# Kernel tuning notes

Measured on AMD Instinct MI355X. Metric: run time of the kernel, lower is better.

Reference implementation:

```python
import jax, jax.numpy as jnp
import numpy as np

B, IN, COND, H, LAT, E, GH = 8192, 256, 1024, 1024, 128, 6, 64
INP = LAT + COND      # decoder layer0 input size = 1152
INTER = LAT + H       # decoder layer1/2 input size = 1152


def setup_inputs() -> dict:
    key = jax.random.key(0)
    ks = jax.random.split(key, 30)
    n = lambda k, shape, s=0.02: jax.random.normal(k, shape, dtype=jnp.float32) * s
    return {
        'x': jax.random.normal(ks[0], (B, IN), dtype=jnp.float32),
        'y': jax.random.normal(ks[1], (B, COND), dtype=jnp.float32),
        'eps': jax.random.normal(ks[2], (B, LAT), dtype=jnp.float32),
        # encoder: layer k input = prev_dim + IN (x is re-concatenated each layer)
        'enc_w0': n(ks[3], (IN + COND + IN, H)), 'enc_b0': jnp.zeros((H,), jnp.float32),
        'enc_w1': n(ks[4], (H + IN, H)),         'enc_b1': jnp.zeros((H,), jnp.float32),
        'mu_w': n(ks[5], (H, LAT)),  'mu_b': jnp.zeros((LAT,), jnp.float32),
        'lv_w': n(ks[6], (H, LAT)),  'lv_b': jnp.zeros((LAT,), jnp.float32),
        # gating network (input = latent + cond)
        'g_w0': n(ks[7], (INP, GH)), 'g_b0': jnp.zeros((GH,), jnp.float32),
        'g_w1': n(ks[8], (GH, GH)),  'g_b1': jnp.zeros((GH,), jnp.float32),
        'g_w2': n(ks[9], (GH, E)),   'g_b2': jnp.zeros((E,), jnp.float32),
        # expert weights [E, in, out] and biases [E, out] (bias init 0.01 as in source)
        'exp_w0': n(ks[10], (E, INP, H)),   'exp_b0': jnp.full((E, H), 0.01, jnp.float32),
        'exp_w1': n(ks[11], (E, INTER, H)), 'exp_b1': jnp.full((E, H), 0.01, jnp.float32),
        'exp_w2': n(ks[12], (E, INTER, IN)), 'exp_b2': jnp.full((E, IN), 0.01, jnp.float32),
    }


def _forward(x, y, eps, enc_w0, enc_b0, enc_w1, enc_b1, mu_w, mu_b, lv_w, lv_b,
             g_w0, g_b0, g_w1, g_b1, g_w2, g_b2,
             exp_w0, exp_b0, exp_w1, exp_b1, exp_w2, exp_b2):
    elu = jax.nn.elu
    # --- Encoder ---
    h = jnp.concatenate([x, y], axis=1)
    h = elu(jnp.concatenate([h, x], axis=1) @ enc_w0 + enc_b0)
    h = elu(jnp.concatenate([h, x], axis=1) @ enc_w1 + enc_b1)
    mu = h @ mu_w + mu_b
    logvar = h @ lv_w + lv_b
    # --- Reparameterize (eps passed explicitly for determinism) ---
    z = mu + eps * jnp.exp(0.5 * logvar)
    # --- MixedDecoder ---
    g = jnp.concatenate([z, y], axis=1)
    g = elu(g @ g_w0 + g_b0)
    g = elu(g @ g_w1 + g_b1)
    coeff = jax.nn.softmax(g @ g_w2 + g_b2, axis=1)  # [B, E]
    layer_out = y
    for W, bb, act in ((exp_w0, exp_b0, True), (exp_w1, exp_b1, True), (exp_w2, exp_b2, False)):
        inp = jnp.concatenate([z, layer_out], axis=1)  # [B, I]
        # fused mixture-of-experts projection: avoids materializing per-sample [B,I,O] weight
        out = coeff @ bb + jnp.einsum('be,bi,eio->bo', coeff, inp, W)
        layer_out = elu(out) if act else out
    return layer_out, mu, logvar


def reference(x, y, eps, enc_w0, enc_b0, enc_w1, enc_b1, mu_w, mu_b, lv_w, lv_b,
              g_w0, g_b0, g_w1, g_b1, g_w2, g_b2,
              exp_w0, exp_b0, exp_w1, exp_b1, exp_w2, exp_b2):
    return _forward(x, y, eps, enc_w0, enc_b0, enc_w1, enc_b1, mu_w, mu_b, lv_w, lv_b,
                    g_w0, g_b0, g_w1, g_b1, g_w2, g_b2,
                    exp_w0, exp_b0, exp_w1, exp_b1, exp_w2, exp_b2)
```

## Files before the change

### kernel.cpp

```cpp
#include <hip/hip_runtime.h>
#include <hip/hip_bf16.h>
#include <cstddef>

using u16 = unsigned short;
using short8 = __attribute__((ext_vector_type(8))) short;
using f32x4 = __attribute__((ext_vector_type(4))) float;

constexpr int B_   = 8192;
constexpr int IN_  = 256;
constexpr int COND_= 1024;
constexpr int H_   = 1024;
constexpr int LAT_ = 128;
constexpr int NE_  = 6;
constexpr int GH_  = 64;
constexpr int INP_ = 1152;
constexpr int K0_  = 1536;
constexpr int K1_  = 1280;

constexpr int BK = 64;

typedef const __attribute__((address_space(1))) void gv_t;
typedef __attribute__((address_space(3))) void lv_t;
#define GLDS(g, l) __builtin_amdgcn_global_load_lds((gv_t*)(g), (lv_t*)(l), 16, 0, 0)

__device__ __forceinline__ u16 f2b(float f) {
  __hip_bfloat16 h = __float2bfloat16(f);
  return *reinterpret_cast<u16*>(&h);
}
__device__ __forceinline__ ushort4 f2b4(float4 v) {
  ushort4 o;
  o.x = f2b(v.x); o.y = f2b(v.y); o.z = f2b(v.z); o.w = f2b(v.w);
  return o;
}
__device__ __forceinline__ float elu1(float x) { return x > 0.f ? x : (__expf(x) - 1.f); }

__global__ void k_transpose(const float* __restrict__ in, u16* __restrict__ out,
                            int R, int C, long inStride, long outStride) {
  __shared__ float t[32][33];
  const float* ip = in + (long)blockIdx.z * inStride;
  u16* op = out + (long)blockIdx.z * outStride;
  int c0 = blockIdx.x * 32, r0 = blockIdx.y * 32;
  int tx = threadIdx.x, ty = threadIdx.y;
#pragma unroll
  for (int i = 0; i < 4; i++) {
    int r = r0 + ty + i * 8, c = c0 + tx;
    if (r < R && c < C) t[ty + i * 8][tx] = ip[(long)r * C + c];
  }
  __syncthreads();
#pragma unroll
  for (int i = 0; i < 4; i++) {
    int c = c0 + ty + i * 8, r = r0 + tx;
    if (r < R && c < C) op[(long)c * R + r] = f2b(t[tx][ty + i * 8]);
  }
}

__global__ __launch_bounds__(256) void k_pre(
    const float* __restrict__ enc_w0, const float* __restrict__ enc_w1,
    const float* __restrict__ mu_w, const float* __restrict__ lv_w,
    const float* __restrict__ g_w0, const float* __restrict__ exp_w0,
    const float* __restrict__ exp_w1,
    const float* __restrict__ x, const float* __restrict__ y,
    u16* __restrict__ encw0T, u16* __restrict__ encw1T, u16* __restrict__ mulvT,
    u16* __restrict__ gw0T, u16* __restrict__ ew0T, u16* __restrict__ ew1T,
    u16* __restrict__ A0, u16* __restrict__ A1, int pbase)
{
  __shared__ float t[32][33];
  const int b = blockIdx.x;
  const int tid = threadIdx.x;
  const int tx = tid & 31, ty = tid >> 5;

  auto tr = [&](const float* in, u16* out, int R, int C, int bx, int by) {
    int c0 = bx * 32, r0 = by * 32;
#pragma unroll
    for (int i = 0; i < 4; i++) {
      int r = r0 + ty + i * 8, c = c0 + tx;
      if (r < R && c < C) t[ty + i * 8][tx] = in[(long)r * C + c];
    }
    __syncthreads();
#pragma unroll
    for (int i = 0; i < 4; i++) {
      int c = c0 + ty + i * 8, r = r0 + tx;
      if (r < R && c < C) out[(long)c * R + r] = f2b(t[tx][ty + i * 8]);
    }
  };

  if (b < 1536)       { tr(enc_w0, encw0T, K0_, H_, b & 31, b >> 5); }
  else if (b < 2816)  { int l = b - 1536; tr(enc_w1, encw1T, K1_, H_, l & 31, l >> 5); }
  else if (b < 2944)  { int l = b - 2816; tr(mu_w, mulvT, H_, LAT_, l & 3, l >> 2); }
  else if (b < 3072)  { int l = b - 2944; tr(lv_w, mulvT + (size_t)LAT_ * H_, H_, LAT_, l & 3, l >> 2); }
  else if (b < 3144)  { int l = b - 3072; tr(g_w0, gw0T, INP_, GH_, l & 1, l >> 1); }
  else if (b < 10056) {
    int l = b - 3144, e = l / 1152, r2 = l % 1152;
    tr(exp_w0 + (long)e * INP_ * H_, ew0T + (long)e * INP_ * H_, INP_, H_, r2 & 31, r2 >> 5);
  } else if (b < pbase) {
    int l = b - 10056, e = l / 1152, r2 = l % 1152;
    tr(exp_w1 + (long)e * INP_ * H_, ew1T + (long)e * INP_ * H_, INP_, H_, r2 & 31, r2 >> 5);
  } else {
    long idx = (long)(b - pbase) * 256 + tid;
    long n0v = (long)B_ * K0_ / 4;
    if (idx < n0v) {
      long base = idx * 4;
      int bb = (int)(base / K0_), c = (int)(base % K0_);
      float4 v;
      if (c < IN_)              v = *(const float4*)&x[(long)bb * IN_ + c];
      else if (c < IN_ + COND_) v = *(const float4*)&y[(long)bb * COND_ + (c - IN_)];
      else                      v = *(const float4*)&x[(long)bb * IN_ + (c - IN_ - COND_)];
      *(ushort4*)&A0[base] = f2b4(v);
    } else {
      long j = idx - n0v;
      if (j < (long)B_ * IN_ / 4) {
        long base = j * 4;
        int bb = (int)(base / IN_), c = (int)(base % IN_);
        float4 v = *(const float4*)&x[(long)bb * IN_ + c];
        *(ushort4*)&A1[(long)bb * K1_ + H_ + c] = f2b4(v);
      }
    }
  }
}

__global__ __launch_bounds__(256) void k_mid(
    const float* __restrict__ exp_w2, u16* __restrict__ ew2T,
    const float* __restrict__ mu, const float* __restrict__ lv,
    const float* __restrict__ eps, const float* __restrict__ y,
    u16* __restrict__ ZY, u16* __restrict__ D1, u16* __restrict__ D2)
{
  __shared__ float t[32][33];
  const int b = blockIdx.x;
  const int tid = threadIdx.x;
  if (b < 1728) {
    const int tx = tid & 31, ty = tid >> 5;
    int e = b / 288, r2 = b % 288;
    const float* in = exp_w2 + (long)e * INP_ * IN_;
    u16* out = ew2T + (long)e * INP_ * IN_;
    int c0 = (r2 & 7) * 32, r0 = (r2 >> 3) * 32;
#pragma unroll
    for (int i = 0; i < 4; i++) {
      int r = r0 + ty + i * 8, c = c0 + tx;
      if (r < INP_ && c < IN_) t[ty + i * 8][tx] = in[(long)r * IN_ + c];
    }
    __syncthreads();
#pragma unroll
    for (int i = 0; i < 4; i++) {
      int c = c0 + ty + i * 8, r = r0 + tx;
      if (r < INP_ && c < IN_) out[(long)c * INP_ + r] = f2b(t[tx][ty + i * 8]);
    }
  } else {
    long idx = (long)(b - 1728) * 256 + tid;
    if (idx >= (long)B_ * INP_ / 4) return;
    long base = idx * 4;
    int bb = (int)(base / INP_), c = (int)(base % INP_);
    if (c < LAT_) {
      long o = (long)bb * LAT_ + c;
      float4 m = *(const float4*)&mu[o];
      float4 l = *(const float4*)&lv[o];
      float4 e4 = *(const float4*)&eps[o];
      float4 z;
      z.x = m.x + e4.x * __expf(0.5f * l.x);
      z.y = m.y + e4.y * __expf(0.5f * l.y);
      z.z = m.z + e4.z * __expf(0.5f * l.z);
      z.w = m.w + e4.w * __expf(0.5f * l.w);
      ushort4 zb = f2b4(z);
      *(ushort4*)&ZY[base] = zb;
      *(ushort4*)&D1[base] = zb;
      *(ushort4*)&D2[base] = zb;
    } else {
      float4 v = *(const float4*)&y[(long)bb * COND_ + (c - LAT_)];
      *(ushort4*)&ZY[base] = f2b4(v);
    }
  }
}

__global__ __launch_bounds__(256) void k_gate(const float* __restrict__ G1,
    const float* __restrict__ w1, const float* __restrict__ b1,
    const float* __restrict__ w2, const float* __restrict__ b2,
    float* __restrict__ coeff) {
  __shared__ float W1[64][65];
  __shared__ float W2[64][8];
  __shared__ float B1[64], B2[8];
  int tid = threadIdx.x;
  for (int i = tid; i < 64 * 64; i += 256) W1[i >> 6][i & 63] = w1[i];
  for (int i = tid; i < 64 * 6; i += 256) W2[i / 6][i % 6] = w2[i];
  if (tid < 64) B1[tid] = b1[tid];
  if (tid < 8)  B2[tid] = (tid < 6) ? b2[tid] : 0.f;
  __syncthreads();
  int row = blockIdx.x * 256 + tid;
  const float* gr = G1 + (long)row * GH_;
  float g[64];
#pragma unroll
  for (int i = 0; i < 16; i++) {
    float4 v = *(const float4*)(gr + i * 4);
    g[i*4] = v.x; g[i*4+1] = v.y; g[i*4+2] = v.z; g[i*4+3] = v.w;
  }
  float lg[6];
#pragma unroll
  for (int e = 0; e < 6; e++) lg[e] = B2[e];
  for (int n = 0; n < 64; n++) {
    float s = B1[n];
#pragma unroll
    for (int k = 0; k < 64; k++) s += g[k] * W1[k][n];
    s = elu1(s);
#pragma unroll
    for (int e = 0; e < 6; e++) lg[e] += s * W2[n][e];
  }
  float m = lg[0];
#pragma unroll
  for (int e = 1; e < 6; e++) m = fmaxf(m, lg[e]);
  float p[6], sum = 0.f;
#pragma unroll
  for (int e = 0; e < 6; e++) { p[e] = __expf(lg[e] - m); sum += p[e]; }
  float inv = 1.f / sum;
#pragma unroll
  for (int e = 0; e < 6; e++) coeff[(long)row * 6 + e] = p[e] * inv;
}

template<int KSTEPS, int E, bool MOE>
__global__ __launch_bounds__(512, 2) void k_gemm8(
    const u16* __restrict__ A,
    const u16* __restrict__ WT,
    const float* __restrict__ bias,
    const float* __restrict__ coeff,
    int N,
    u16* __restrict__ outH, int ldo)
{
  constexpr int KK = KSTEPS * BK;
  constexpr int T = E * KSTEPS;
  __shared__ __align__(16) u16 As[3][256][BK];
  __shared__ __align__(16) u16 Bs[3][128][BK];
  __shared__ float Cf[MOE ? 256 : 1][8];

  const int tid = threadIdx.x;
  const int lane = tid & 63, w = tid >> 6;
  const int wr = w >> 1, wc = w & 1;
  const int lin = blockIdx.x + blockIdx.y * gridDim.x;
  const int rb  = (lin & 7) * 4 + ((lin >> 3) & 3);
  const int cp  = lin >> 5;
  const int brow = rb * 256, bcol = cp * 128;
  const int lr = lane & 15, hi = lane >> 4;
  const int lk = hi * 8;
  const int xsw = (lr & 7) << 3;

  if (MOE) {
    if (tid < 256) {
#pragma unroll
      for (int e2 = 0; e2 < 8; e2++)
        Cf[tid][e2] = (e2 < 6) ? coeff[(long)(brow + tid) * 6 + e2] : 0.f;
    }
    __syncthreads();
  }

  f32x4 acc[4][4];
#pragma unroll
  for (int m = 0; m < 4; m++)
#pragma unroll
    for (int n = 0; n < 4; n++)
#pragma unroll
      for (int r = 0; r < 4; r++) acc[m][n][r] = 0.f;
  f32x4 pacc[MOE ? 4 : 1][MOE ? 4 : 1];
  if constexpr (MOE) {
#pragma unroll
    for (int m = 0; m < 4; m++)
#pragma unroll
      for (int n = 0; n < 4; n++)
#pragma unroll
        for (int r = 0; r < 4; r++) pacc[m][n][r] = 0.f;
  }

  const int srow = w * 8 + (lane >> 3);
  const int sdst = (lane & 7) * 8;
  const int ssrc = ((lane & 7) ^ ((lane >> 3) & 7)) * 8;
  const u16* Asrc = A + (long)(brow + srow) * KK + ssrc;
  const u16* Bsrc = WT + (long)(bcol + srow) * KK + ssrc;

  auto STAGE_H = [&](int t2, int buf, int h) {
    const int e2 = (E == 1) ? 0 : (t2 / KSTEPS);
    int k2 = (E == 1) ? t2 : (t2 % KSTEPS);
    if (E > 1 && (e2 & 1)) k2 = KSTEPS - 1 - k2;
    const u16* ap = Asrc + (long)k2 * BK;
    const u16* bp = Bsrc + (long)e2 * ((long)N * KK) + (long)k2 * BK;
    GLDS(ap + (long)((h * 2 + 0) * 64) * KK, &As[buf][(h * 2 + 0) * 64 + srow][sdst]);
    GLDS(ap + (long)((h * 2 + 1) * 64) * KK, &As[buf][(h * 2 + 1) * 64 + srow][sdst]);
    GLDS(bp + (long)(h * 64) * KK,           &Bs[buf][h * 64 + srow][sdst]);
  };

  STAGE_H(0, 0, 0); STAGE_H(0, 0, 1);
  STAGE_H(1, 1, 0); STAGE_H(1, 1, 1);
  asm volatile("s_waitcnt vmcnt(6)" ::: "memory");
  asm volatile("s_barrier" ::: "memory");

  for (int t = 0; t < T; ++t) {
    const int cur = t % 3;
    const int nbuf = (t + 2) % 3;
    const bool do_stage = (t + 2 < T);

    {
      short8 af[4], bfr[4];
      const int cc = lk ^ xsw;
#pragma unroll
      for (int m = 0; m < 4; m++)
        af[m] = *(const short8*)&As[cur][wr * 64 + m * 16 + lr][cc];
#pragma unroll
      for (int n = 0; n < 4; n++)
        bfr[n] = *(const short8*)&Bs[cur][wc * 64 + n * 16 + lr][cc];
      if (do_stage) STAGE_H(t + 2, nbuf, 0);
      asm volatile("s_barrier" ::: "memory");
      __builtin_amdgcn_s_setprio(1);
#pragma unroll
      for (int m = 0; m < 4; m++)
#pragma unroll
        for (int n = 0; n < 4; n++) {
          if constexpr (MOE)
            pacc[m][n] = __builtin_amdgcn_mfma_f32_16x16x32_bf16(af[m], bfr[n], pacc[m][n], 0, 0, 0);
          else
            acc[m][n] = __builtin_amdgcn_mfma_f32_16x16x32_bf16(af[m], bfr[n], acc[m][n], 0, 0, 0);
        }
      __builtin_amdgcn_s_setprio(0);
      asm volatile("s_barrier" ::: "memory");
    }

    {
      short8 af[4], bfr[4];
      const int cc = (32 + lk) ^ xsw;
#pragma unroll
      for (int m = 0; m < 4; m++)
        af[m] = *(const short8*)&As[cur][wr * 64 + m * 16 + lr][cc];
#pragma unroll
      for (int n = 0; n < 4; n++)
        bfr[n] = *(const short8*)&Bs[cur][wc * 64 + n * 16 + lr][cc];
      if (do_stage) STAGE_H(t + 2, nbuf, 1);
      asm volatile("s_barrier" ::: "memory");
      __builtin_amdgcn_s_setprio(1);
#pragma unroll
      for (int m = 0; m < 4; m++)
#pragma unroll
        for (int n = 0; n < 4; n++) {
          if constexpr (MOE)
            pacc[m][n] = __builtin_amdgcn_mfma_f32_16x16x32_bf16(af[m], bfr[n], pacc[m][n], 0, 0, 0);
          else
            acc[m][n] = __builtin_amdgcn_mfma_f32_16x16x32_bf16(af[m], bfr[n], acc[m][n], 0, 0, 0);
        }
      __builtin_amdgcn_s_setprio(0);
      if (t + 1 < T) {
        if (do_stage) asm volatile("s_waitcnt vmcnt(6)" ::: "memory");
        else          asm volatile("s_waitcnt vmcnt(0)" ::: "memory");
      }
      asm volatile("s_barrier" ::: "memory");
    }

    if constexpr (MOE) {
      if ((t + 1) % KSTEPS == 0) {
        const int e = t / KSTEPS;
#pragma unroll
        for (int m = 0; m < 4; m++)
#pragma unroll
          for (int r = 0; r < 4; r++) {
            float c = Cf[wr * 64 + m * 16 + hi * 4 + r][e];
#pragma unroll
            for (int n = 0; n < 4; n++) acc[m][n][r] += c * pacc[m][n][r];
          }
        if (t + 1 < T) {
#pragma unroll
          for (int m = 0; m < 4; m++)
#pragma unroll
            for (int n = 0; n < 4; n++)
#pragma unroll
              for (int r = 0; r < 4; r++) pacc[m][n][r] = 0.f;
        }
      }
    }
  }

#pragma unroll
  for (int m = 0; m < 4; m++)
#pragma unroll
    for (int n = 0; n < 4; n++) {
      const int col = bcol + wc * 64 + n * 16 + lr;
#pragma unroll
      for (int r = 0; r < 4; r++) {
        const int rowl = wr * 64 + m * 16 + hi * 4 + r;
        const long row = brow + rowl;
        float v = acc[m][n][r];
        if constexpr (MOE) {
          float bv = 0.f;
#pragma unroll
          for (int e = 0; e < 6; e++) bv += Cf[rowl][e] * bias[(long)e * N + col];
          v += bv;
        } else {
          v += bias[col];
        }
        v = elu1(v);
        outH[row * (long)ldo + col] = f2b(v);
      }
    }
}

template<int KSTEPS, int E, bool MOE>
__global__ __launch_bounds__(256, 2) void k_m2(
    const u16* __restrict__ A,
    const u16* __restrict__ WT,
    const float* __restrict__ bias, const float* __restrict__ bias2,
    const float* __restrict__ coeff,
    int N,
    u16* __restrict__ outH, float* __restrict__ outF, float* __restrict__ outF2,
    int ldo, int splitcol, int act)
{
  constexpr int KK = KSTEPS * BK;
  constexpr int T = E * KSTEPS;
  __shared__ __align__(16) u16 As[3][64][BK];
  __shared__ __align__(16) u16 Bs[3][128][BK];
  __shared__ float Cf[MOE ? 64 : 1][8];

  const int tid = threadIdx.x;
  const int lane = tid & 63, w = tid >> 6;
  const int wr = w >> 1, wc = w & 1;
  const int brow = blockIdx.x * 64, bcol = blockIdx.y * 128;
  const int lr = lane & 15, hi = lane >> 4;
  const int lk = hi * 8;
  const int xsw = (lr & 7) << 3;

  if (MOE) {
    if (tid < 64) {
#pragma unroll
      for (int e2 = 0; e2 < 8; e2++)
        Cf[tid][e2] = (e2 < 6) ? coeff[(long)(brow + tid) * 6 + e2] : 0.f;
    }
    __syncthreads();
  }

  f32x4 acc[2][4];
#pragma unroll
  for (int m = 0; m < 2; m++)
#pragma unroll
    for (int n = 0; n < 4; n++)
#pragma unroll
      for (int r = 0; r < 4; r++) acc[m][n][r] = 0.f;
  f32x4 pacc[MOE ? 2 : 1][MOE ? 4 : 1];
  if constexpr (MOE) {
#pragma unroll
    for (int m = 0; m < 2; m++)
#pragma unroll
      for (int n = 0; n < 4; n++)
#pragma unroll
        for (int r = 0; r < 4; r++) pacc[m][n][r] = 0.f;
  }

  const int srow = w * 8 + (lane >> 3);
  const int sdst = (lane & 7) * 8;
  const int ssrc = ((lane & 7) ^ ((lane >> 3) & 7)) * 8;
  const u16* Asrc = A + (long)(brow + srow) * KK + ssrc;
  const u16* Bsrc = WT + (long)(bcol + srow) * KK + ssrc;

  auto STAGE_H = [&](int t2, int buf, int h) {
    const int e2 = (E == 1) ? 0 : (t2 / KSTEPS);
    int k2 = (E == 1) ? t2 : (t2 % KSTEPS);
    if (E > 1 && (e2 & 1)) k2 = KSTEPS - 1 - k2;
    const u16* ap = Asrc + (long)k2 * BK;
    const u16* bp = Bsrc + (long)e2 * ((long)N * KK) + (long)k2 * BK;
    GLDS(ap + (long)(h * 32) * KK,            &As[buf][h * 32 + srow][sdst]);
    GLDS(bp + (long)(h * 64) * KK,            &Bs[buf][h * 64 + srow][sdst]);
    GLDS(bp + (long)(h * 64 + 32) * KK,       &Bs[buf][h * 64 + 32 + srow][sdst]);
  };

  STAGE_H(0, 0, 0); STAGE_H(0, 0, 1);
  STAGE_H(1, 1, 0); STAGE_H(1, 1, 1);
  asm volatile("s_waitcnt vmcnt(6)" ::: "memory");
  asm volatile("s_barrier" ::: "memory");

  for (int t = 0; t < T; ++t) {
    const int cur = t % 3;
    const int nbuf = (t + 2) % 3;
    const bool do_stage = (t + 2 < T);

    {
      short8 af[2], bfr[4];
      const int cc = lk ^ xsw;
#pragma unroll
      for (int m = 0; m < 2; m++)
        af[m] = *(const short8*)&As[cur][wr * 32 + m * 16 + lr][cc];
#pragma unroll
      for (int n = 0; n < 4; n++)
        bfr[n] = *(const short8*)&Bs[cur][wc * 64 + n * 16 + lr][cc];
      if (do_stage) STAGE_H(t + 2, nbuf, 0);
      asm volatile("s_barrier" ::: "memory");
      __builtin_amdgcn_s_setprio(1);
#pragma unroll
      for (int m = 0; m < 2; m++)
#pragma unroll
        for (int n = 0; n < 4; n++) {
          if constexpr (MOE)
            pacc[m][n] = __builtin_amdgcn_mfma_f32_16x16x32_bf16(af[m], bfr[n], pacc[m][n], 0, 0, 0);
          else
            acc[m][n] = __builtin_amdgcn_mfma_f32_16x16x32_bf16(af[m], bfr[n], acc[m][n], 0, 0, 0);
        }
      __builtin_amdgcn_s_setprio(0);
      asm volatile("s_barrier" ::: "memory");
    }
    {
      short8 af[2], bfr[4];
      const int cc = (32 + lk) ^ xsw;
#pragma unroll
      for (int m = 0; m < 2; m++)
        af[m] = *(const short8*)&As[cur][wr * 32 + m * 16 + lr][cc];
#pragma unroll
      for (int n = 0; n < 4; n++)
        bfr[n] = *(const short8*)&Bs[cur][wc * 64 + n * 16 + lr][cc];
      if (do_stage) STAGE_H(t + 2, nbuf, 1);
      asm volatile("s_barrier" ::: "memory");
      __builtin_amdgcn_s_setprio(1);
#pragma unroll
      for (int m = 0; m < 2; m++)
#pragma unroll
        for (int n = 0; n < 4; n++) {
          if constexpr (MOE)
            pacc[m][n] = __builtin_amdgcn_mfma_f32_16x16x32_bf16(af[m], bfr[n], pacc[m][n], 0, 0, 0);
          else
            acc[m][n] = __builtin_amdgcn_mfma_f32_16x16x32_bf16(af[m], bfr[n], acc[m][n], 0, 0, 0);
        }
      __builtin_amdgcn_s_setprio(0);
      if (t + 1 < T) {
        if (do_stage) asm volatile("s_waitcnt vmcnt(6)" ::: "memory");
        else          asm volatile("s_waitcnt vmcnt(0)" ::: "memory");
      }
      asm volatile("s_barrier" ::: "memory");
    }

    if constexpr (MOE) {
      if ((t + 1) % KSTEPS == 0) {
        const int e = t / KSTEPS;
#pragma unroll
        for (int m = 0; m < 2; m++)
#pragma unroll
          for (int r = 0; r < 4; r++) {
            float c = Cf[wr * 32 + m * 16 + hi * 4 + r][e];
#pragma unroll
            for (int n = 0; n < 4; n++) acc[m][n][r] += c * pacc[m][n][r];
          }
        if (t + 1 < T) {
#pragma unroll
          for (int m = 0; m < 2; m++)
#pragma unroll
            for (int n = 0; n < 4; n++)
#pragma unroll
              for (int r = 0; r < 4; r++) pacc[m][n][r] = 0.f;
        }
      }
    }
  }

#pragma unroll
  for (int m = 0; m < 2; m++)
#pragma unroll
    for (int n = 0; n < 4; n++) {
      const int col = bcol + wc * 64 + n * 16 + lr;
      if (col >= N) continue;
#pragma unroll
      for (int r = 0; r < 4; r++) {
        const int rowl = wr * 32 + m * 16 + hi * 4 + r;
        const long row = brow + rowl;
        float v = acc[m][n][r];
        if constexpr (MOE) {
          float bv = 0.f;
#pragma unroll
          for (int e = 0; e < 6; e++) bv += Cf[rowl][e] * bias[(long)e * N + col];
          v += bv;
        } else {
          v += (col < splitcol) ? bias[col] : bias2[col - splitcol];
        }
        if (act) v = elu1(v);
        if (outH) outH[row * (long)ldo + col] = f2b(v);
        else if (col < splitcol) outF[row * (long)ldo + col] = v;
        else outF2[row * (long)ldo + (col - splitcol)] = v;
      }
    }
}

extern "C" void kernel_launch(void* const* d_in, const int* in_sizes, int n_in,
                              void* d_out, int out_size, void* d_ws, size_t ws_size,
                              hipStream_t stream) {
  (void)in_sizes; (void)out_size;
  if (n_in < 23) return;
  const float* x      = (const float*)d_in[0];
  const float* y      = (const float*)d_in[1];
  const float* eps    = (const float*)d_in[2];
  const float* enc_w0 = (const float*)d_in[3];
  const float* enc_b0 = (const float*)d_in[4];
  const float* enc_w1 = (const float*)d_in[5];
  const float* enc_b1 = (const float*)d_in[6];
  const float* mu_w   = (const float*)d_in[7];
  const float* mu_b   = (const float*)d_in[8];
  const float* lv_w   = (const float*)d_in[9];
  const float* lv_b   = (const float*)d_in[10];
  const float* g_w0   = (const float*)d_in[11];
  const float* g_b0   = (const float*)d_in[12];
  const float* g_w1   = (const float*)d_in[13];
  const float* g_b1   = (const float*)d_in[14];
  const float* g_w2   = (const float*)d_in[15];
  const float* g_b2   = (const float*)d_in[16];
  const float* exp_w0 = (const float*)d_in[17];
  const float* exp_b0 = (const float*)d_in[18];
  const float* exp_w1 = (const float*)d_in[19];
  const float* exp_b1 = (const float*)d_in[20];
  const float* exp_w2 = (const float*)d_in[21];
  const float* exp_b2 = (const float*)d_in[22];

  char* ws = (char*)d_ws;
  size_t off = 0;
  auto alloc = [&](size_t bytes) -> void* {
    void* p = ws + off; off += (bytes + 255) & ~(size_t)255; return p;
  };
  u16* A0     = (u16*)alloc((size_t)B_ * K0_ * 2);
  u16* A1     = (u16*)alloc((size_t)B_ * K1_ * 2);
  u16* H2     = (u16*)alloc((size_t)B_ * H_ * 2);
  u16* ZY     = (u16*)alloc((size_t)B_ * INP_ * 2);
  u16* encw0T = (u16*)alloc((size_t)K0_ * H_ * 2);
  u16* encw1T = (u16*)alloc((size_t)K1_ * H_ * 2);
  u16* mulvT  = (u16*)alloc((size_t)256 * H_ * 2);
  u16* gw0T   = (u16*)alloc((size_t)GH_ * INP_ * 2);
  u16* ew0T   = (u16*)alloc((size_t)NE_ * H_ * INP_ * 2);
  if (ws_size < off) return;

  size_t ew1_bytes = (size_t)NE_ * H_ * INP_ * 2;
  u16* ew1T_sep = nullptr;
  if (off + ew1_bytes <= ws_size) ew1T_sep = (u16*)alloc(ew1_bytes);

  u16* D1 = A0;
  u16* D2 = A1;
  float* G1    = (float*)H2;
  float* COEFF = (float*)((char*)H2 + (size_t)B_ * GH_ * 4);
  u16* ew2T = (u16*)((char*)H2 + (size_t)4 * 1024 * 1024);
  u16* ew1T = ew1T_sep ? ew1T_sep : ZY;

  float* outO = (float*)d_out;
  float* muO  = outO + (size_t)B_ * IN_;
  float* lvO  = muO + (size_t)B_ * LAT_;

  const int hoist = ew1T_sep ? 1 : 0;
  const int pbase = hoist ? 16968 : 10056;
  const int pre_grid = pbase + 14336;

  k_pre<<<pre_grid, 256, 0, stream>>>(enc_w0, enc_w1, mu_w, lv_w, g_w0, exp_w0,
      exp_w1, x, y, encw0T, encw1T, mulvT, gw0T, ew0T, ew1T, A0, A1, pbase);

  k_gemm8<K0_ / BK, 1, false><<<dim3(32, 8), 512, 0, stream>>>(A0, encw0T, enc_b0,
      nullptr, H_, A1, K1_);
  k_gemm8<K1_ / BK, 1, false><<<dim3(32, 8), 512, 0, stream>>>(A1, encw1T, enc_b1,
      nullptr, H_, H2, H_);

  k_m2<H_ / BK, 1, false><<<dim3(B_ / 64, 2), 256, 0, stream>>>(H2, mulvT,
      mu_b, lv_b, nullptr, 256, nullptr, muO, lvO, LAT_, LAT_, 0);

  k_mid<<<10944, 256, 0, stream>>>(exp_w2, ew2T, muO, lvO, eps, y, ZY, D1, D2);

  k_m2<INP_ / BK, 1, false><<<dim3(B_ / 64, 1), 256, 0, stream>>>(ZY, gw0T,
      g_b0, g_b0, nullptr, GH_, nullptr, G1, nullptr, GH_, GH_, 1);
  k_gate<<<B_ / 256, 256, 0, stream>>>(G1, g_w1, g_b1, g_w2, g_b2, COEFF);

  k_gemm8<INP_ / BK, NE_, true><<<dim3(32, 8), 512, 0, stream>>>(ZY, ew0T, exp_b0,
      COEFF, H_, D1 + LAT_, INP_);
  if (!hoist) {
    k_transpose<<<dim3(32, 36, NE_), dim3(32, 8), 0, stream>>>(exp_w1, ew1T, INP_, H_,
                                                      (long)INP_ * H_, (long)INP_ * H_);
  }
  k_gemm8<INP_ / BK, NE_, true><<<dim3(32, 8), 512, 0, stream>>>(D1, ew1T, exp_b1,
      COEFF, H_, D2 + LAT_, INP_);
  k_m2<INP_ / BK, NE_, true><<<dim3(B_ / 64, 2), 256, 0, stream>>>(D2, ew2T,
      exp_b2, nullptr, COEFF, IN_, nullptr, outO, nullptr, IN_, IN_, 0);
}
```

Measured before the change: 521.6 us.

## Add dedicated MoE GEMM kernel with k-outer expert-inner loop and A-tile reuse

Introduces k_moe4, a 256-thread kernel with 128x128 tiles for the two large mixture-of-experts layers. The loop runs over K outermost and all six experts inside, so one A tile is loaded into shared memory once and reused across experts. Each expert's partial product is scaled by its gate coefficient and added to the accumulator at every K step. This removes the repeated A reloads per expert in the old expert-outer order, at the cost of more per-step coefficient FMAs, smaller tiles and more blocks. The encoder GEMM is simplified to a non-MoE-only template.

```diff
diff --git a/kernel.cpp b/kernel.cpp
--- a/kernel.cpp
+++ b/kernel.cpp
@@ -213,8 +213,8 @@
   for (int e = 0; e < 6; e++) coeff[(long)row * 6 + e] = p[e] * inv;
 }
 
-template<int KSTEPS, int E, bool MOE>
-__global__ __launch_bounds__(512, 2) void k_gemm8(
+template<int KSTEPS>
+__global__ __launch_bounds__(256, 2) void k_moe4(
     const u16* __restrict__ A,
     const u16* __restrict__ WT,
     const float* __restrict__ bias,
@@ -223,10 +223,167 @@
     u16* __restrict__ outH, int ldo)
 {
   constexpr int KK = KSTEPS * BK;
-  constexpr int T = E * KSTEPS;
+  constexpr int T = NE_ * KSTEPS;
+  __shared__ __align__(16) u16 As[128][BK];
+  __shared__ __align__(16) u16 Bs[3][128][BK];
+  __shared__ float Cf[128][8];
+
+  const int tid = threadIdx.x;
+  const int lane = tid & 63, w = tid >> 6;
+  const int wr = w >> 1, wc = w & 1;
+  const int lin = blockIdx.x + blockIdx.y * gridDim.x;
+  const int rb  = (lin & 7) * 8 + ((lin >> 3) & 7);
+  const int cp  = lin >> 6;
+  const int brow = rb * 128, bcol = cp * 128;
+  const int lr = lane & 15, hi = lane >> 4;
+  const int lk = hi * 8;
+  const int xsw = (lr & 7) << 3;
+
+  if (tid < 128) {
+#pragma unroll
+    for (int e2 = 0; e2 < 8; e2++)
+      Cf[tid][e2] = (e2 < 6) ? coeff[(long)(brow + tid) * 6 + e2] : 0.f;
+  }
+  __syncthreads();
+
+  f32x4 acc[4][4];
+#pragma unroll
+  for (int m = 0; m < 4; m++)
+#pragma unroll
+    for (int n = 0; n < 4; n++)
+#pragma unroll
+      for (int r = 0; r < 4; r++) acc[m][n][r] = 0.f;
+  const f32x4 zf = {0.f, 0.f, 0.f, 0.f};
+  f32x4 pacc[4][4];
+
+  const int srow = w * 8 + (lane >> 3);
+  const int sdst = (lane & 7) * 8;
+  const int ssrc = ((lane & 7) ^ ((lane >> 3) & 7)) * 8;
+  const u16* Asrc = A + (long)(brow + srow) * KK + ssrc;
+  const u16* Bsrc = WT + (long)(bcol + srow) * KK + ssrc;
+
+  auto STAGE_A = [&](int kt2) {
+    const u16* ap = Asrc + (long)kt2 * BK;
+#pragma unroll
+    for (int i = 0; i < 4; i++)
+      GLDS(ap + (long)(i * 32) * KK, &As[i * 32 + srow][sdst]);
+  };
+  auto STAGE_B = [&](int s2) {
+    const int kt2 = s2 / NE_, e2 = s2 % NE_;
+    const u16* bp = Bsrc + (long)e2 * ((long)N * KK) + (long)kt2 * BK;
+#pragma unroll
+    for (int i = 0; i < 4; i++)
+      GLDS(bp + (long)(i * 32) * KK, &Bs[s2 % 3][i * 32 + srow][sdst]);
+  };
+
+  STAGE_A(0);
+  STAGE_B(0);
+  STAGE_B(1);
+  asm volatile("s_waitcnt vmcnt(4)" ::: "memory");
+  asm volatile("s_barrier" ::: "memory");
+
+  short8 af[2][4];
+
+  for (int kt = 0; kt < KSTEPS; ++kt) {
+    const bool haveA = (kt + 1 < KSTEPS);
+#pragma unroll
+    for (int g = 0; g < NE_; ++g) {
+      const int s = kt * NE_ + g;
+      const int cur = s % 3;
+      const bool stageB = (s + 2 < T);
+
+      {
+        if (g == 0) {
+#pragma unroll
+          for (int p = 0; p < 2; p++)
+#pragma unroll
+            for (int m = 0; m < 4; m++)
+              af[p][m] = *(const short8*)&As[wr * 64 + m * 16 + lr][(p * 32 + lk) ^ xsw];
+        }
+        short8 bfr[4];
+        const int cc0 = lk ^ xsw;
+#pragma unroll
+        for (int n = 0; n < 4; n++)
+          bfr[n] = *(const short8*)&Bs[cur][wc * 64 + n * 16 + lr][cc0];
+        if (stageB) STAGE_B(s + 2);
+        if (g == 1 && haveA) STAGE_A(kt + 1);
+        asm volatile("s_barrier" ::: "memory");
+        __builtin_amdgcn_s_setprio(1);
+#pragma unroll
+        for (int m = 0; m < 4; m++)
+#pragma unroll
+          for (int n = 0; n < 4; n++)
+            pacc[m][n] = __builtin_amdgcn_mfma_f32_16x16x32_bf16(af[0][m], bfr[n], zf, 0, 0, 0);
+        __builtin_amdgcn_s_setprio(0);
+        asm volatile("s_barrier" ::: "memory");
+      }
+      {
+        short8 bfr[4];
+        const int cc1 = (32 + lk) ^ xsw;
+#pragma unroll
+        for (int n = 0; n < 4; n++)
+          bfr[n] = *(const short8*)&Bs[cur][wc * 64 + n * 16 + lr][cc1];
+        asm volatile("s_barrier" ::: "memory");
+        __builtin_amdgcn_s_setprio(1);
+#pragma unroll
+        for (int m = 0; m < 4; m++)
+#pragma unroll
+          for (int n = 0; n < 4; n++)
+            pacc[m][n] = __builtin_amdgcn_mfma_f32_16x16x32_bf16(af[1][m], bfr[n], pacc[m][n], 0, 0, 0);
+        __builtin_amdgcn_s_setprio(0);
+        if (stageB) {
+          if ((g == 1 || g == 2) && haveA)
+            asm volatile("s_waitcnt vmcnt(8)" ::: "memory");
+          else
+            asm volatile("s_waitcnt vmcnt(4)" ::: "memory");
+        } else {
+          asm volatile("s_waitcnt vmcnt(0)" ::: "memory");
+        }
+        asm volatile("s_barrier" ::: "memory");
+      }
+#pragma unroll
+      for (int m = 0; m < 4; m++)
+#pragma unroll
+        for (int r = 0; r < 4; r++) {
+          const float c = Cf[wr * 64 + m * 16 + hi * 4 + r][g];
+#pragma unroll
+          for (int n = 0; n < 4; n++) acc[m][n][r] += c * pacc[m][n][r];
+        }
+    }
+  }
+
+#pragma unroll
+  for (int m = 0; m < 4; m++)
+#pragma unroll
+    for (int n = 0; n < 4; n++) {
+      const int col = bcol + wc * 64 + n * 16 + lr;
+#pragma unroll
+      for (int r = 0; r < 4; r++) {
+        const int rowl = wr * 64 + m * 16 + hi * 4 + r;
+        const long row = brow + rowl;
+        float v = acc[m][n][r];
+        float bv = 0.f;
+#pragma unroll
+        for (int e = 0; e < 6; e++) bv += Cf[rowl][e] * bias[(long)e * N + col];
+        v += bv;
+        v = elu1(v);
+        outH[row * (long)ldo + col] = f2b(v);
+      }
+    }
+}
+
+template<int KSTEPS>
+__global__ __launch_bounds__(512, 2) void k_gemm8(
+    const u16* __restrict__ A,
+    const u16* __restrict__ WT,
+    const float* __restrict__ bias,
+    int N,
+    u16* __restrict__ outH, int ldo)
+{
+  constexpr int KK = KSTEPS * BK;
+  constexpr int T = KSTEPS;
   __shared__ __align__(16) u16 As[3][256][BK];
   __shared__ __align__(16) u16 Bs[3][128][BK];
-  __shared__ float Cf[MOE ? 256 : 1][8];
 
   const int tid = threadIdx.x;
   const int lane = tid & 63, w = tid >> 6;
@@ -239,15 +396,6 @@
   const int lk = hi * 8;
   const int xsw = (lr & 7) << 3;
 
-  if (MOE) {
-    if (tid < 256) {
-#pragma unroll
-      for (int e2 = 0; e2 < 8; e2++)
-        Cf[tid][e2] = (e2 < 6) ? coeff[(long)(brow + tid) * 6 + e2] : 0.f;
-    }
-    __syncthreads();
-  }
-
   f32x4 acc[4][4];
 #pragma unroll
   for (int m = 0; m < 4; m++)
@@ -255,15 +403,6 @@
     for (int n = 0; n < 4; n++)
 #pragma unroll
       for (int r = 0; r < 4; r++) acc[m][n][r] = 0.f;
-  f32x4 pacc[MOE ? 4 : 1][MOE ? 4 : 1];
-  if constexpr (MOE) {
-#pragma unroll
-    for (int m = 0; m < 4; m++)
-#pragma unroll
-      for (int n = 0; n < 4; n++)
-#pragma unroll
-        for (int r = 0; r < 4; r++) pacc[m][n][r] = 0.f;
-  }
 
   const int srow = w * 8 + (lane >> 3);
   const int sdst = (lane & 7) * 8;
@@ -272,11 +411,8 @@
   const u16* Bsrc = WT + (long)(bcol + srow) * KK + ssrc;
 
   auto STAGE_H = [&](int t2, int buf, int h) {
-    const int e2 = (E == 1) ? 0 : (t2 / KSTEPS);
-    int k2 = (E == 1) ? t2 : (t2 % KSTEPS);
-    if (E > 1 && (e2 & 1)) k2 = KSTEPS - 1 - k2;
-    const u16* ap = Asrc + (long)k2 * BK;
-    const u16* bp = Bsrc + (long)e2 * ((long)N * KK) + (long)k2 * BK;
+    const u16* ap = Asrc + (long)t2 * BK;
+    const u16* bp = Bsrc + (long)t2 * BK;
     GLDS(ap + (long)((h * 2 + 0) * 64) * KK, &As[buf][(h * 2 + 0) * 64 + srow][sdst]);
     GLDS(ap + (long)((h * 2 + 1) * 64) * KK, &As[buf][(h * 2 + 1) * 64 + srow][sdst]);
     GLDS(bp + (long)(h * 64) * KK,           &Bs[buf][h * 64 + srow][sdst]);
@@ -307,16 +443,11 @@
 #pragma unroll
       for (int m = 0; m < 4; m++)
 #pragma unroll
-        for (int n = 0; n < 4; n++) {
-          if constexpr (MOE)
-            pacc[m][n] = __builtin_amdgcn_mfma_f32_16x16x32_bf16(af[m], bfr[n], pacc[m][n], 0, 0, 0);
-          else
-            acc[m][n] = __builtin_amdgcn_mfma_f32_16x16x32_bf16(af[m], bfr[n], acc[m][n], 0, 0, 0);
-        }
+        for (int n = 0; n < 4; n++)
+          acc[m][n] = __builtin_amdgcn_mfma_f32_16x16x32_bf16(af[m], bfr[n], acc[m][n], 0, 0, 0);
       __builtin_amdgcn_s_setprio(0);
       asm volatile("s_barrier" ::: "memory");
     }
-
     {
       short8 af[4], bfr[4];
       const int cc = (32 + lk) ^ xsw;
@@ -332,12 +463,8 @@
 #pragma unroll
       for (int m = 0; m < 4; m++)
 #pragma unroll
-        for (int n = 0; n < 4; n++) {
-          if constexpr (MOE)
-            pacc[m][n] = __builtin_amdgcn_mfma_f32_16x16x32_bf16(af[m], bfr[n], pacc[m][n], 0, 0, 0);
-          else
-            acc[m][n] = __builtin_amdgcn_mfma_f32_16x16x32_bf16(af[m], bfr[n], acc[m][n], 0, 0, 0);
-        }
+        for (int n = 0; n < 4; n++)
+          acc[m][n] = __builtin_amdgcn_mfma_f32_16x16x32_bf16(af[m], bfr[n], acc[m][n], 0, 0, 0);
       __builtin_amdgcn_s_setprio(0);
       if (t + 1 < T) {
         if (do_stage) asm volatile("s_waitcnt vmcnt(6)" ::: "memory");
@@ -345,28 +472,6 @@
       }
       asm volatile("s_barrier" ::: "memory");
     }
-
-    if constexpr (MOE) {
-      if ((t + 1) % KSTEPS == 0) {
-        const int e = t / KSTEPS;
-#pragma unroll
-        for (int m = 0; m < 4; m++)
-#pragma unroll
-          for (int r = 0; r < 4; r++) {
-            float c = Cf[wr * 64 + m * 16 + hi * 4 + r][e];
-#pragma unroll
-            for (int n = 0; n < 4; n++) acc[m][n][r] += c * pacc[m][n][r];
-          }
-        if (t + 1 < T) {
-#pragma unroll
-          for (int m = 0; m < 4; m++)
-#pragma unroll
-            for (int n = 0; n < 4; n++)
-#pragma unroll
-              for (int r = 0; r < 4; r++) pacc[m][n][r] = 0.f;
-        }
-      }
-    }
   }
 
 #pragma unroll
@@ -378,15 +483,7 @@
       for (int r = 0; r < 4; r++) {
         const int rowl = wr * 64 + m * 16 + hi * 4 + r;
         const long row = brow + rowl;
-        float v = acc[m][n][r];
-        if constexpr (MOE) {
-          float bv = 0.f;
-#pragma unroll
-          for (int e = 0; e < 6; e++) bv += Cf[rowl][e] * bias[(long)e * N + col];
-          v += bv;
-        } else {
-          v += bias[col];
-        }
+        float v = acc[m][n][r] + bias[col];
         v = elu1(v);
         outH[row * (long)ldo + col] = f2b(v);
       }
@@ -640,10 +737,8 @@
   k_pre<<<pre_grid, 256, 0, stream>>>(enc_w0, enc_w1, mu_w, lv_w, g_w0, exp_w0,
       exp_w1, x, y, encw0T, encw1T, mulvT, gw0T, ew0T, ew1T, A0, A1, pbase);
 
-  k_gemm8<K0_ / BK, 1, false><<<dim3(32, 8), 512, 0, stream>>>(A0, encw0T, enc_b0,
-      nullptr, H_, A1, K1_);
-  k_gemm8<K1_ / BK, 1, false><<<dim3(32, 8), 512, 0, stream>>>(A1, encw1T, enc_b1,
-      nullptr, H_, H2, H_);
+  k_gemm8<K0_ / BK><<<dim3(32, 8), 512, 0, stream>>>(A0, encw0T, enc_b0, H_, A1, K1_);
+  k_gemm8<K1_ / BK><<<dim3(32, 8), 512, 0, stream>>>(A1, encw1T, enc_b1, H_, H2, H_);
 
   k_m2<H_ / BK, 1, false><<<dim3(B_ / 64, 2), 256, 0, stream>>>(H2, mulvT,
       mu_b, lv_b, nullptr, 256, nullptr, muO, lvO, LAT_, LAT_, 0);
@@ -654,13 +749,13 @@
       g_b0, g_b0, nullptr, GH_, nullptr, G1, nullptr, GH_, GH_, 1);
   k_gate<<<B_ / 256, 256, 0, stream>>>(G1, g_w1, g_b1, g_w2, g_b2, COEFF);
 
-  k_gemm8<INP_ / BK, NE_, true><<<dim3(32, 8), 512, 0, stream>>>(ZY, ew0T, exp_b0,
+  k_moe4<INP_ / BK><<<dim3(64, 8), 256, 0, stream>>>(ZY, ew0T, exp_b0,
       COEFF, H_, D1 + LAT_, INP_);
   if (!hoist) {
     k_transpose<<<dim3(32, 36, NE_), dim3(32, 8), 0, stream>>>(exp_w1, ew1T, INP_, H_,
                                                       (long)INP_ * H_, (long)INP_ * H_);
   }
-  k_gemm8<INP_ / BK, NE_, true><<<dim3(32, 8), 512, 0, stream>>>(D1, ew1T, exp_b1,
+  k_moe4<INP_ / BK><<<dim3(64, 8), 256, 0, stream>>>(D1, ew1T, exp_b1,
       COEFF, H_, D2 + LAT_, INP_);
   k_m2<INP_ / BK, NE_, true><<<dim3(B_ / 64, 2), 256, 0, stream>>>(D2, ew2T,
       exp_b2, nullptr, COEFF, IN_, nullptr, outO, nullptr, IN_, IN_, 0);
```

Measured after the change: 714.0 us. +36.9%, slower.
